# Kernel tuning notes

Hardware: AMD Instinct MI355X
Metric: run time of the kernel (lower is better)

Reference implementation:

```python
import math
import jax, jax.numpy as jnp
import numpy as np

HEAD_DIM = 64


def skew(X):
    # X: (B, M, L). Pad M+1 zeros on last dim, flatten, drop last M, reshape.
    # Shifts row i right by i -> aligns relative positions (adaptive-span trick).
    B, M, L = X.shape
    X = jnp.pad(X, ((0, 0), (0, 0), (0, M + 1)))  # (B, M, L+M+1)
    X = X.reshape(B, -1)[:, :-M].reshape(B, M, M + L)
    return X


def setup_inputs() -> dict:
    key = jax.random.key(0)
    k1, k2, k3, k4 = jax.random.split(key, 4)
    BH, M, D, LIM = 16, 2048, HEAD_DIM, 2048
    return {
        "query": jax.random.normal(k1, (BH, M, D), jnp.float32),
        "key": jax.random.normal(k2, (BH, M, D), jnp.float32),
        "value": jax.random.normal(k3, (BH, M, D), jnp.float32),
        "key_pe": jax.random.normal(k4, (1, D, LIM), jnp.float32),
    }


def reference(query, key, value, key_pe):
    M = query.shape[1]
    Lk = key.shape[1]
    neg_inf = jnp.float32(float("-inf"))
    # causal mask: -inf strictly above diagonal, last M rows
    mask_causal = jnp.triu(jnp.full((Lk, Lk), neg_inf, dtype=query.dtype), k=1)[-M:]
    # content scores: (BH, M, Lk)
    attn = jnp.einsum("bmd,bld->bml", query, key)
    L_size = attn.shape[-1]
    # relative-position scores via skew trick
    attn_pos = jnp.einsum("bmd,xdl->bml", query, key_pe[:, :, -L_size:])
    attn_pos = skew(attn_pos)[:, :, -L_size - 1:-1]
    attn = (attn + attn_pos + mask_causal) / math.sqrt(HEAD_DIM)
    attn = jax.nn.softmax(attn, axis=-1)
    out = jnp.einsum("bml,bld->bmd", attn, value)
    return out  # aux_loss is the constant 0 in the original module
```

## Files before the change

kernel.cpp:

```cpp
#include <hip/hip_runtime.h>
#include <hip/hip_bf16.h>

typedef __attribute__((ext_vector_type(8))) short short8;
typedef __attribute__((ext_vector_type(4))) float f32x4;

#define MFMA16(A, B, C) __builtin_amdgcn_mfma_f32_16x16x32_bf16((A), (B), (C), 0, 0, 0)

#define GL16(gp, lp) __builtin_amdgcn_global_load_lds( \
    (const __attribute__((address_space(1))) void*)(gp), \
    (__attribute__((address_space(3))) void*)(lp), 16, 0, 0)

__device__ __forceinline__ unsigned short bfbits(float f) {
  return __builtin_bit_cast(unsigned short, (__bf16)f);
}

constexpr int BH = 16;
constexpr int Mn = 2048;
constexpr int Dn = 64;
constexpr int LIMn = 2048;
constexpr size_t KF_SHORTS = (size_t)BH * 32 * 8 * 512;
constexpr size_t PE_JROWS = 132;
constexpr size_t PEF_SHORTS = PE_JROWS * 2 * 512;
constexpr int PART_SLOT = 4224;
constexpr int SLOTS_PER_HEAD = 72;

__device__ __forceinline__ int part_offs(int mt) {
  return (mt < 16) ? 2 * (mt - 8) : (mt < 24 ? 16 + 3 * (mt - 16) : 40 + 4 * (mt - 24));
}


__global__ void prep_all(const float* __restrict__ K, const float* __restrict__ V,
                         const float* __restrict__ PE,
                         unsigned short* __restrict__ Kf, unsigned short* __restrict__ Vf,
                         unsigned short* __restrict__ PEf) {
  __shared__ float tA[64 * 64];
  __shared__ float tB[64 * 64];
  const int b = blockIdx.x, tid = threadIdx.x;
  const int w = tid >> 6, lane = tid & 63, g = lane >> 4, q15 = lane & 15;

  if (b < 512) {
    const int bh = b >> 5, lt = b & 31;
    const float* Ks = K + ((size_t)bh * Mn + lt * 64) * Dn;
    const float* Vs = V + ((size_t)bh * Mn + lt * 64) * Dn;
    const int row = tid >> 2, c0 = (tid & 3) * 16;
#pragma unroll
    for (int i = 0; i < 4; ++i) {
      *(float4*)&tA[row * 64 + c0 + 4 * i] = ((const float4*)(Ks + (size_t)row * 64 + c0))[i];
      *(float4*)&tB[row * 64 + c0 + 4 * i] = ((const float4*)(Vs + (size_t)row * 64 + c0))[i];
    }
    __syncthreads();
#pragma unroll
    for (int i = 0; i < 2; ++i) {
      const int f = 2 * w + i, nt = f >> 1, s = f & 1;
      short8 uk, uv;
#pragma unroll
      for (int j = 0; j < 8; ++j) {
        uk[j] = (short)bfbits(tA[(nt * 16 + q15) * 64 + s * 32 + g * 8 + j]);
        uv[j] = (short)bfbits(tB[(s * 32 + g * 8 + j) * 64 + nt * 16 + q15]);
      }
      const size_t base = ((size_t)(bh * 32 + lt) * 8 + f) * 512 + lane * 8;
      *(short8*)&Kf[base] = uk;
      *(short8*)&Vf[base] = uv;
    }
  } else {
    const int pb = b - 512;
    const int c0 = pb * 64;
    const int d = tid >> 2, cc = (tid & 3) * 16;
#pragma unroll
    for (int i = 0; i < 16; ++i) {
      const int c = c0 + cc + i;
      tA[(cc + i) * 64 + d] = (c < LIMn) ? PE[(size_t)d * LIMn + c] : 0.0f;
    }
    __syncthreads();
#pragma unroll
    for (int s = 0; s < 2; ++s) {
      short8 u;
#pragma unroll
      for (int j = 0; j < 8; ++j)
        u[j] = (short)bfbits(tA[(w * 16 + q15) * 64 + s * 32 + g * 8 + j]);
      *(short8*)&PEf[((size_t)(4 * pb + w) * 2 + s) * 512 + lane * 8] = u;
    }
  }
}


__launch_bounds__(256)
__global__ void stair_main(const float* __restrict__ Qg,
                           const unsigned short* __restrict__ Kf,
                           const unsigned short* __restrict__ Vf,
                           const unsigned short* __restrict__ PEf,
                           float* __restrict__ Og,
                           float* __restrict__ Part,
                           int split) {
  __shared__ __align__(16) unsigned short Kbuf[2][2][4096];
  __shared__ __align__(16) unsigned short Vbuf[2][2][4096];
  __shared__ __align__(16) unsigned short Plds[4][2048];

  const int tid = threadIdx.x;
  const int w = tid >> 6, lane = tid & 63, g = lane >> 4, q15 = lane & 15;
  const int bid = blockIdx.x;

  int bh, mt, chunk, t0, t1, nch;
  bh = bid & 15;
  if (split) {
    const int u = bid >> 4;
    if (u < 32)      { mt = 31 - (u >> 2); chunk = u & 3; }
    else if (u < 56) { const int v = u - 32, q = v / 3; mt = 23 - q; chunk = v - q * 3; }
    else if (u < 72) { const int v = u - 56; mt = 15 - (v >> 1); chunk = v & 1; }
    else             { mt = 7 - (u - 72); chunk = 0; }
    t0 = chunk * 8;
    t1 = (t0 + 8 < mt + 1) ? (t0 + 8) : (mt + 1);
    nch = (mt + 8) >> 3;
  } else {
    mt = 31 - (bid >> 4); chunk = 0; t0 = 0; t1 = mt + 1; nch = 1;
  }
  const int m0w = mt * 64 + w * 16;
  const int jb0 = 127 - 4 * mt - w;

  const float* Qb = Qg + (size_t)bh * Mn * Dn;
  float* Ob = Og + (size_t)bh * Mn * Dn;

  short8 aq[2];
  {
    const float* qp = Qb + (size_t)(m0w + q15) * Dn;
#pragma unroll
    for (int s = 0; s < 2; ++s) {
      const float4* p = (const float4*)(qp + s * 32 + g * 8);
      float4 f0 = p[0], f1 = p[1];
      short8 a;
      a[0]=(short)bfbits(f0.x); a[1]=(short)bfbits(f0.y); a[2]=(short)bfbits(f0.z); a[3]=(short)bfbits(f0.w);
      a[4]=(short)bfbits(f1.x); a[5]=(short)bfbits(f1.y); a[6]=(short)bfbits(f1.z); a[7]=(short)bfbits(f1.w);
      aq[s] = a;
    }
  }

  float mrun[4], lp[4];
  f32x4 o[4] = {};
#pragma unroll
  for (int r = 0; r < 4; ++r) { mrun[r] = -1e30f; lp[r] = 0.0f; }

  auto STAGE1 = [&](int b, int slot, int t) {
    const size_t toff = ((size_t)(bh * 32 + t) * 8) * 512;
#pragma unroll
    for (int i = 0; i < 2; ++i) {
      const int f = 2 * w + i;
      const size_t off = toff + (size_t)f * 512 + lane * 8;
      GL16(&Kf[off], &Kbuf[b][slot][f * 512]);
      GL16(&Vf[off], &Vbuf[b][slot][f * 512]);
    }
  };

  auto QK = [&](f32x4 qk[4], int cur, int slot, int ntmax) {
#pragma unroll
    for (int s = 0; s < 2; ++s)
#pragma unroll
      for (int nt = 0; nt < 4; ++nt)
        if (nt <= ntmax) {
          short8 bfr = *(const short8*)&Kbuf[cur][slot][(nt * 2 + s) * 512 + lane * 8];
          qk[nt] = MFMA16(aq[s], bfr, qk[nt]);
        }
  };

  auto GATHER = [&](float sv[4][4], const f32x4 qk[4], const f32x4 ev[5],
                    int ntmax, bool diag) {
#pragma unroll
    for (int nt = 0; nt < 4; ++nt)
      if (nt <= ntmax) {
#pragma unroll
        for (int r = 0; r < 4; ++r) {
          const int rw = g * 4 + r;
          const int srcLane = (lane & 48) | ((q15 + 15 - rw) & 15);
          const bool cond = (((q15 + rw + 1) & 15) > rw);
          const float sel = cond ? ev[nt + 1][r] : ev[nt][r];
          const float er = __shfl(sel, srcLane, 64);
          const int li = nt * 16 + q15;
          const bool masked = diag && (li > w * 16 + rw);
          sv[nt][r] = masked ? -1e30f : (qk[nt][r] + er) * 0.125f;
        }
      }
  };

  auto PV = [&](const float sv[4][4], int cur, int slot, int smax) {
#pragma unroll
    for (int nt = 0; nt < 4; ++nt)
#pragma unroll
      for (int r = 0; r < 4; ++r) {
        const int rw = g * 4 + r;
        Plds[w][slot * 1024 + ((rw * 64 + nt * 16 + q15) ^ ((rw & 7) << 3))] = bfbits(sv[nt][r]);
      }
    short8 pa[2];
#pragma unroll
    for (int s = 0; s < 2; ++s)
      if (s <= smax)
        pa[s] = *(short8*)&Plds[w][slot * 1024 + ((q15 * 64 + s * 32 + g * 8) ^ ((q15 & 7) << 3))];
#pragma unroll
    for (int s = 0; s < 2; ++s)
      if (s <= smax)
#pragma unroll
        for (int nt = 0; nt < 4; ++nt) {
          short8 bfr = *(const short8*)&Vbuf[cur][slot][(nt * 2 + s) * 512 + lane * 8];
          o[nt] = MFMA16(pa[s], bfr, o[nt]);
        }
  };

  auto PAIR = [&](int t, int cur, bool diagB) {
    const int jbA = jb0 + 4 * t;
    const int jbB = jbA + 4;
    const int ntmaxB = diagB ? w : 3;
    const int u5B = diagB ? (w + 2) : 5;
    const int smaxB = diagB ? (w >> 1) : 1;

    short8 peA[2][5], peB[2][5];
#pragma unroll
    for (int s = 0; s < 2; ++s)
#pragma unroll
      for (int u = 0; u < 5; ++u) {
        peA[s][u] = *(const short8*)&PEf[((size_t)(jbA + u) * 2 + s) * 512 + lane * 8];
        if (u < u5B)
          peB[s][u] = *(const short8*)&PEf[((size_t)(jbB + u) * 2 + s) * 512 + lane * 8];
      }

    f32x4 qkA[4] = {}, qkB[4] = {};
    QK(qkA, cur, 0, 3);
    QK(qkB, cur, 1, ntmaxB);

    f32x4 evA[5] = {};
#pragma unroll
    for (int s = 0; s < 2; ++s)
#pragma unroll
      for (int u = 0; u < 5; ++u) evA[u] = MFMA16(aq[s], peA[s][u], evA[u]);

    float svA[4][4], svB[4][4];
#pragma unroll
    for (int nt = 0; nt < 4; ++nt)
#pragma unroll
      for (int r = 0; r < 4; ++r) { svA[nt][r] = -1e30f; svB[nt][r] = -1e30f; }

    GATHER(svA, qkA, evA, 3, false);

    f32x4 evB[5] = {};
#pragma unroll
    for (int s = 0; s < 2; ++s)
#pragma unroll
      for (int u = 0; u < 5; ++u)
        if (u < u5B) evB[u] = MFMA16(aq[s], peB[s][u], evB[u]);

    GATHER(svB, qkB, evB, ntmaxB, diagB);

    float lmax[4];
#pragma unroll
    for (int r = 0; r < 4; ++r) {
      float a = fmaxf(fmaxf(svA[0][r], svA[1][r]), fmaxf(svA[2][r], svA[3][r]));
      float b = fmaxf(fmaxf(svB[0][r], svB[1][r]), fmaxf(svB[2][r], svB[3][r]));
      lmax[r] = fmaxf(a, b);
    }
    const bool fast = __all((lmax[0] <= mrun[0] + 8.f) & (lmax[1] <= mrun[1] + 8.f) &
                            (lmax[2] <= mrun[2] + 8.f) & (lmax[3] <= mrun[3] + 8.f));
    if (!fast) {
#pragma unroll
      for (int r = 0; r < 4; ++r) {
        float mx = lmax[r];
        mx = fmaxf(mx, __shfl_xor(mx, 1));
        mx = fmaxf(mx, __shfl_xor(mx, 2));
        mx = fmaxf(mx, __shfl_xor(mx, 4));
        mx = fmaxf(mx, __shfl_xor(mx, 8));
        const float mn = fmaxf(mrun[r], mx);
        const float alpha = exp2f((mrun[r] - mn) * 1.44269504f);
        mrun[r] = mn;
        lp[r] *= alpha;
        o[0][r] *= alpha; o[1][r] *= alpha; o[2][r] *= alpha; o[3][r] *= alpha;
      }
    }
#pragma unroll
    for (int nt = 0; nt < 4; ++nt)
#pragma unroll
      for (int r = 0; r < 4; ++r) {
        svA[nt][r] = exp2f((svA[nt][r] - mrun[r]) * 1.44269504f);
        svB[nt][r] = exp2f((svB[nt][r] - mrun[r]) * 1.44269504f);
      }
#pragma unroll
    for (int r = 0; r < 4; ++r)
      lp[r] += ((svA[0][r] + svA[1][r]) + (svA[2][r] + svA[3][r])) +
               ((svB[0][r] + svB[1][r]) + (svB[2][r] + svB[3][r]));

    PV(svA, cur, 0, 1);
    PV(svB, cur, 1, smaxB);
  };

  auto SINGLE = [&](int t, int cur, bool diag) {
    const int jb = jb0 + 4 * t;
    const int ntmax = diag ? w : 3;
    const int u5 = diag ? (w + 2) : 5;
    const int smax = diag ? (w >> 1) : 1;

    short8 pe[2][5];
#pragma unroll
    for (int s = 0; s < 2; ++s)
#pragma unroll
      for (int u = 0; u < 5; ++u)
        if (u < u5)
          pe[s][u] = *(const short8*)&PEf[((size_t)(jb + u) * 2 + s) * 512 + lane * 8];

    f32x4 qk[4] = {};
    QK(qk, cur, 0, ntmax);
    f32x4 ev[5] = {};
#pragma unroll
    for (int s = 0; s < 2; ++s)
#pragma unroll
      for (int u = 0; u < 5; ++u)
        if (u < u5) ev[u] = MFMA16(aq[s], pe[s][u], ev[u]);

    float sv[4][4];
#pragma unroll
    for (int nt = 0; nt < 4; ++nt)
#pragma unroll
      for (int r = 0; r < 4; ++r) sv[nt][r] = -1e30f;
    GATHER(sv, qk, ev, ntmax, diag);

    float lmax[4];
#pragma unroll
    for (int r = 0; r < 4; ++r)
      lmax[r] = fmaxf(fmaxf(sv[0][r], sv[1][r]), fmaxf(sv[2][r], sv[3][r]));
    const bool fast = __all((lmax[0] <= mrun[0] + 8.f) & (lmax[1] <= mrun[1] + 8.f) &
                            (lmax[2] <= mrun[2] + 8.f) & (lmax[3] <= mrun[3] + 8.f));
    if (!fast) {
#pragma unroll
      for (int r = 0; r < 4; ++r) {
        float mx = lmax[r];
        mx = fmaxf(mx, __shfl_xor(mx, 1));
        mx = fmaxf(mx, __shfl_xor(mx, 2));
        mx = fmaxf(mx, __shfl_xor(mx, 4));
        mx = fmaxf(mx, __shfl_xor(mx, 8));
        const float mn = fmaxf(mrun[r], mx);
        const float alpha = exp2f((mrun[r] - mn) * 1.44269504f);
        mrun[r] = mn;
        lp[r] *= alpha;
        o[0][r] *= alpha; o[1][r] *= alpha; o[2][r] *= alpha; o[3][r] *= alpha;
      }
    }
#pragma unroll
    for (int nt = 0; nt < 4; ++nt)
#pragma unroll
      for (int r = 0; r < 4; ++r)
// ... 8 lines not shown
    int cur = 0;
    int t = t0;
    const int n0 = (t1 - t0 >= 2) ? 2 : 1;
    STAGE1(0, 0, t0);
    if (n0 == 2) STAGE1(0, 1, t0 + 1);
    __syncthreads();
    while (t < t1) {
      const int n = (t1 - t >= 2) ? 2 : 1;
      const int rem = t1 - (t + n);
      const int nn = (rem >= 2) ? 2 : rem;
      if (nn > 0) {
        STAGE1(cur ^ 1, 0, t + n);
        if (nn == 2) STAGE1(cur ^ 1, 1, t + n + 1);
      }
      if (n == 2) PAIR(t, cur, (t + 1 == mt));
      else SINGLE(t, cur, (t == mt));
      if (nn > 0) __syncthreads();
      cur ^= 1;
      t += n;
    }
  }

  float lr[4];
#pragma unroll
  for (int r = 0; r < 4; ++r) {
    float s = lp[r];
    s += __shfl_xor(s, 1);
    s += __shfl_xor(s, 2);
    s += __shfl_xor(s, 4);
    s += __shfl_xor(s, 8);
    lr[r] = s;
  }

  if (nch == 1) {
#pragma unroll
    for (int nt = 0; nt < 4; ++nt)
#pragma unroll
      for (int r = 0; r < 4; ++r) {
        const int m = m0w + g * 4 + r;
        Ob[(size_t)m * Dn + nt * 16 + q15] = o[nt][r] / lr[r];
      }
  } else {
    float* ps = Part + ((size_t)bh * SLOTS_PER_HEAD + part_offs(mt) + chunk) * PART_SLOT;
#pragma unroll
    for (int nt = 0; nt < 4; ++nt)
#pragma unroll
      for (int r = 0; r < 4; ++r)
        ps[(w * 16 + g * 4 + r) * 64 + nt * 16 + q15] = o[nt][r];
#pragma unroll
    for (int r = 0; r < 4; ++r)
      if (q15 == g * 4 + r) {
        ps[4096 + w * 16 + q15] = mrun[r];
        ps[4160 + w * 16 + q15] = lr[r];
      }
  }
}


__launch_bounds__(256, 4)
__global__ void combine_parts(const float* __restrict__ Part, float* __restrict__ Og) {
  const int bid = blockIdx.x;
  const int bh = bid & 15;
  const int mt = 8 + (bid >> 4);
  const int nch = (mt + 8) >> 3;
  const float* base = Part + ((size_t)bh * SLOTS_PER_HEAD + part_offs(mt)) * PART_SLOT;
  const int tid = threadIdx.x;
  const int row = tid >> 2;
  const int qc = (tid & 3) * 16;

  float mstar = -1e30f;
#pragma unroll
  for (int c = 0; c < 4; ++c)
    if (c < nch) mstar = fmaxf(mstar, base[c * PART_SLOT + 4096 + row]);
  float lsum = 0.f;
  f32x4 acc0 = {}, acc1 = {}, acc2 = {}, acc3 = {};
#pragma unroll
  for (int c = 0; c < 4; ++c)
    if (c < nch) {
      const float* ps = base + c * PART_SLOT;
      const float sc = exp2f((ps[4096 + row] - mstar) * 1.44269504f);
      lsum += ps[4160 + row] * sc;
      const f32x4* op = (const f32x4*)&ps[row * 64 + qc];
      acc0 += op[0] * sc; acc1 += op[1] * sc; acc2 += op[2] * sc; acc3 += op[3] * sc;
    }
  const float inv = 1.f / lsum;
  float* dst = Og + ((size_t)bh * Mn + mt * 64 + row) * Dn + qc;
  *(f32x4*)&dst[0]  = acc0 * inv;
  *(f32x4*)&dst[4]  = acc1 * inv;
  *(f32x4*)&dst[8]  = acc2 * inv;
  *(f32x4*)&dst[12] = acc3 * inv;
}


constexpr int ESTRIDE = 84;

__launch_bounds__(256, 2)
__global__ void stair_attn_fb(const float* __restrict__ Qg,
                              const float* __restrict__ Kg,
                              const float* __restrict__ Vg,
                              const float* __restrict__ PEg,
                              float* __restrict__ Og) {
  __shared__ __align__(16) unsigned short Kb[64 * 64];
  __shared__ __align__(16) unsigned short Vt[64 * 64];
  __shared__ __align__(16) unsigned short Pb[128 * 64];
  __shared__ __align__(16) float Elds[4 * 16 * ESTRIDE];
  __shared__ __align__(16) unsigned short Plds[4 * 16 * 64];

  const int tid = threadIdx.x;
  const int w = tid >> 6;
  const int lane = tid & 63;
  const int g = lane >> 4;
  const int q15 = lane & 15;

  const int bid = blockIdx.x;
  const int bh = bid & 15;
  const int jid = bid >> 4;
  const int mt = (jid < 16) ? (2 * jid) : (63 - 2 * jid);
  const int m0 = mt * 64;

  const float* Qb = Qg + (size_t)bh * Mn * Dn;
  const float* Kbase = Kg + (size_t)bh * Mn * Dn;
  const float* Vbase = Vg + (size_t)bh * Mn * Dn;
  float* Ob = Og + (size_t)bh * Mn * Dn;
// ... 173 lines not shown
    for (int s = 0; s < 2; ++s)
#pragma unroll
      for (int nt = 0; nt < 4; ++nt) {
        int d = nt * 16 + q15;
        short8 b = *(short8*)&Vt[(d * 64 + s * 32 + dso) ^ ((d & 7) << 3)];
        o[nt] = MFMA16(pa[s], b, o[nt]);
      }
  }

#pragma unroll
  for (int nt = 0; nt < 4; ++nt)
#pragma unroll
    for (int r = 0; r < 4; ++r) {
      int m = m0 + 16 * w + g * 4 + r;
      Ob[(size_t)m * Dn + nt * 16 + q15] = o[nt][r] / lrun[r];
    }
}


extern "C" void kernel_launch(void* const* d_in, const int* in_sizes, int n_in,
                              void* d_out, int out_size, void* d_ws, size_t ws_size,
                              hipStream_t stream) {
  (void)in_sizes; (void)n_in; (void)out_size;
  const float* Q  = (const float*)d_in[0];
  const float* K  = (const float*)d_in[1];
  const float* V  = (const float*)d_in[2];
  const float* PE = (const float*)d_in[3];
  float* Out = (float*)d_out;

  const size_t szK = KF_SHORTS * sizeof(unsigned short);
  const size_t szV = szK;
  const size_t szP = PEF_SHORTS * sizeof(unsigned short);
  const size_t szPart = (size_t)BH * SLOTS_PER_HEAD * PART_SLOT * 4;
  const size_t need1 = szK + szV + szP;
  const size_t need2 = need1 + szPart;

  if (ws_size >= need1) {
    unsigned short* Kf  = (unsigned short*)d_ws;
    unsigned short* Vf  = (unsigned short*)((char*)d_ws + szK);
    unsigned short* PEf = (unsigned short*)((char*)d_ws + szK + szV);
    float* Part = (float*)((char*)d_ws + need1);

    hipLaunchKernelGGL(prep_all, dim3(512 + 33), dim3(256), 0, stream, K, V, PE, Kf, Vf, PEf);
    if (ws_size >= need2) {
      hipLaunchKernelGGL(stair_main, dim3(BH * 80), dim3(256), 0, stream,
                         Q, Kf, Vf, PEf, Out, Part, 1);
      hipLaunchKernelGGL(combine_parts, dim3(BH * 24), dim3(256), 0, stream, Part, Out);
    } else {
      hipLaunchKernelGGL(stair_main, dim3(512), dim3(256), 0, stream,
                         Q, Kf, Vf, PEf, Out, (float*)d_ws, 0);
    }
  } else {
    hipLaunchKernelGGL(stair_attn_fb, dim3(512), dim3(256), 0, stream, Q, K, V, PE, Out);
  }
}
```

Before: 75.82 us.

## Precompute skewed positional scores in a separate kernel and stream them as fp16

```diff
diff --git a/kernel.cpp b/kernel.cpp
--- a/kernel.cpp
+++ b/kernel.cpp
@@ -12,6 +12,12 @@
 
 __device__ __forceinline__ unsigned short bfbits(float f) {
   return __builtin_bit_cast(unsigned short, (__bf16)f);
+}
+__device__ __forceinline__ unsigned short h16bits(float f) {
+  return __builtin_bit_cast(unsigned short, (_Float16)f);
+}
+__device__ __forceinline__ float h16val(unsigned short u) {
+  return (float)__builtin_bit_cast(_Float16, u);
 }
 
 constexpr int BH = 16;
@@ -23,6 +29,7 @@
 constexpr size_t PEF_SHORTS = PE_JROWS * 2 * 512;
 constexpr int PART_SLOT = 4224;
 constexpr int SLOTS_PER_HEAD = 72;
+constexpr int TILES_PER_HEAD = 528;
 
 __device__ __forceinline__ int part_offs(int mt) {
   return (mt < 16) ? 2 * (mt - 8) : (mt < 24 ? 16 + 3 * (mt - 16) : 40 + 4 * (mt - 24));
@@ -80,6 +87,351 @@
         u[j] = (short)bfbits(tA[(w * 16 + q15) * 64 + s * 32 + g * 8 + j]);
       *(short8*)&PEf[((size_t)(4 * pb + w) * 2 + s) * 512 + lane * 8] = u;
     }
+  }
+}
+
+
+__launch_bounds__(256)
+__global__ void pos_gemm(const float* __restrict__ Qg,
+                         const unsigned short* __restrict__ PEf,
+                         unsigned short* __restrict__ Spos) {
+  const int tid = threadIdx.x;
+  const int w = tid >> 6, lane = tid & 63, g = lane >> 4, q15 = lane & 15;
+  const int bid = blockIdx.x;
+  const int bh = bid & 15;
+  const int u = bid >> 4;
+  int mt = (int)((sqrtf(8.f * u + 1.f) - 1.f) * 0.5f);
+  while ((mt + 1) * (mt + 2) / 2 <= u) ++mt;
+  while (mt * (mt + 1) / 2 > u) --mt;
+  const int t = u - mt * (mt + 1) / 2;
+  const int m0w = mt * 64 + w * 16;
+  const int jb = 127 - 4 * mt - w + 4 * t;
+
+  short8 aq[2];
+  {
+    const float* qp = Qg + (size_t)bh * Mn * Dn + (size_t)(m0w + q15) * Dn;
+#pragma unroll
+    for (int s = 0; s < 2; ++s) {
+      const float4* p = (const float4*)(qp + s * 32 + g * 8);
+      float4 f0 = p[0], f1 = p[1];
+      short8 a;
+      a[0]=(short)bfbits(f0.x); a[1]=(short)bfbits(f0.y); a[2]=(short)bfbits(f0.z); a[3]=(short)bfbits(f0.w);
+      a[4]=(short)bfbits(f1.x); a[5]=(short)bfbits(f1.y); a[6]=(short)bfbits(f1.z); a[7]=(short)bfbits(f1.w);
+      aq[s] = a;
+    }
+  }
+
+  short8 pe[2][5];
+#pragma unroll
+  for (int s = 0; s < 2; ++s)
+#pragma unroll
+    for (int u5 = 0; u5 < 5; ++u5)
+      pe[s][u5] = *(const short8*)&PEf[((size_t)(jb + u5) * 2 + s) * 512 + lane * 8];
+
+  f32x4 ev[5] = {};
+#pragma unroll
+  for (int s = 0; s < 2; ++s)
+#pragma unroll
+    for (int u5 = 0; u5 < 5; ++u5)
+      ev[u5] = MFMA16(aq[s], pe[s][u5], ev[u5]);
+
+  short8 o0, o1;
+#pragma unroll
+  for (int nt = 0; nt < 4; ++nt)
+#pragma unroll
+    for (int r = 0; r < 4; ++r) {
+      const int rw = g * 4 + r;
+      const int srcLane = (lane & 48) | ((q15 + 15 - rw) & 15);
+      const bool cond = (((q15 + rw + 1) & 15) > rw);
+      const float sel = cond ? ev[nt + 1][r] : ev[nt][r];
+      const float er = __shfl(sel, srcLane, 64);
+      const int idx = nt * 4 + r;
+      if (idx < 8) o0[idx] = (short)h16bits(er);
+      else o1[idx - 8] = (short)h16bits(er);
+    }
+  unsigned short* dst = Spos + (((size_t)(bh * TILES_PER_HEAD + u) * 4 + w) * 64 + lane) * 16;
+  *(short8*)&dst[0] = o0;
+  *(short8*)&dst[8] = o1;
+}
+
+
+__launch_bounds__(256)
+__global__ void stair_main_sp(const float* __restrict__ Qg,
+                              const unsigned short* __restrict__ Kf,
+                              const unsigned short* __restrict__ Vf,
+                              const unsigned short* __restrict__ Spos,
+                              float* __restrict__ Og,
+                              float* __restrict__ Part) {
+  __shared__ __align__(16) unsigned short Kbuf[2][2][4096];
+  __shared__ __align__(16) unsigned short Vbuf[2][2][4096];
+  __shared__ __align__(16) unsigned short Plds[4][2048];
+
+  const int tid = threadIdx.x;
+  const int w = tid >> 6, lane = tid & 63, g = lane >> 4, q15 = lane & 15;
+  const int bid = blockIdx.x;
+
+  int bh, mt, chunk, t0, t1, nch;
+  bh = bid & 15;
+  {
+    const int u = bid >> 4;
+    if (u < 32)      { mt = 31 - (u >> 2); chunk = u & 3; }
+    else if (u < 56) { const int v = u - 32, q = v / 3; mt = 23 - q; chunk = v - q * 3; }
+    else if (u < 72) { const int v = u - 56; mt = 15 - (v >> 1); chunk = v & 1; }
+    else             { mt = 7 - (u - 72); chunk = 0; }
+    t0 = chunk * 8;
+    t1 = (t0 + 8 < mt + 1) ? (t0 + 8) : (mt + 1);
+    nch = (mt + 8) >> 3;
+  }
+  const int m0w = mt * 64 + w * 16;
+  const size_t spBase = ((size_t)bh * TILES_PER_HEAD + (size_t)mt * (mt + 1) / 2);
+
+  const float* Qb = Qg + (size_t)bh * Mn * Dn;
+  float* Ob = Og + (size_t)bh * Mn * Dn;
+
+  short8 aq[2];
+  {
+    const float* qp = Qb + (size_t)(m0w + q15) * Dn;
+#pragma unroll
+    for (int s = 0; s < 2; ++s) {
+      const float4* p = (const float4*)(qp + s * 32 + g * 8);
+      float4 f0 = p[0], f1 = p[1];
+      short8 a;
+      a[0]=(short)bfbits(f0.x); a[1]=(short)bfbits(f0.y); a[2]=(short)bfbits(f0.z); a[3]=(short)bfbits(f0.w);
+      a[4]=(short)bfbits(f1.x); a[5]=(short)bfbits(f1.y); a[6]=(short)bfbits(f1.z); a[7]=(short)bfbits(f1.w);
+      aq[s] = a;
+    }
+  }
+
+  float mrun[4], lp[4];
+  f32x4 o[4] = {};
+#pragma unroll
+  for (int r = 0; r < 4; ++r) { mrun[r] = -1e30f; lp[r] = 0.0f; }
+
+  auto STAGE1 = [&](int b, int slot, int t) {
+    const size_t toff = ((size_t)(bh * 32 + t) * 8) * 512;
+#pragma unroll
+    for (int i = 0; i < 2; ++i) {
+      const int f = 2 * w + i;
+      const size_t off = toff + (size_t)f * 512 + lane * 8;
+      GL16(&Kf[off], &Kbuf[b][slot][f * 512]);
+      GL16(&Vf[off], &Vbuf[b][slot][f * 512]);
+    }
+  };
+
+  auto QK = [&](f32x4 qk[4], int cur, int slot, int ntmax) {
+#pragma unroll
+    for (int s = 0; s < 2; ++s)
+#pragma unroll
+      for (int nt = 0; nt < 4; ++nt)
+        if (nt <= ntmax) {
+          short8 bfr = *(const short8*)&Kbuf[cur][slot][(nt * 2 + s) * 512 + lane * 8];
+          qk[nt] = MFMA16(aq[s], bfr, qk[nt]);
+        }
+  };
+
+  auto PV = [&](const float sv[4][4], int cur, int slot, int smax) {
+#pragma unroll
+    for (int nt = 0; nt < 4; ++nt)
+#pragma unroll
+      for (int r = 0; r < 4; ++r) {
+        const int rw = g * 4 + r;
+        Plds[w][slot * 1024 + ((rw * 64 + nt * 16 + q15) ^ ((rw & 7) << 3))] = bfbits(sv[nt][r]);
+      }
+    short8 pa[2];
+#pragma unroll
+    for (int s = 0; s < 2; ++s)
+      if (s <= smax)
+        pa[s] = *(short8*)&Plds[w][slot * 1024 + ((q15 * 64 + s * 32 + g * 8) ^ ((q15 & 7) << 3))];
+#pragma unroll
+    for (int s = 0; s < 2; ++s)
+      if (s <= smax)
+#pragma unroll
+        for (int nt = 0; nt < 4; ++nt) {
+          short8 bfr = *(const short8*)&Vbuf[cur][slot][(nt * 2 + s) * 512 + lane * 8];
+          o[nt] = MFMA16(pa[s], bfr, o[nt]);
+        }
+  };
+
+  auto PAIR = [&](int t, int cur, bool diagB) {
+    const int ntmaxB = diagB ? w : 3;
+    const int smaxB = diagB ? (w >> 1) : 1;
+
+    const unsigned short* spA = Spos + (((spBase + t) * 4 + w) * 64 + lane) * 16;
+    short8 eA0 = *(const short8*)&spA[0];
+    short8 eA1 = *(const short8*)&spA[8];
+    short8 eB0 = *(const short8*)&spA[4096];
+    short8 eB1 = *(const short8*)&spA[4096 + 8];
+
+    f32x4 qkA[4] = {}, qkB[4] = {};
+    QK(qkA, cur, 0, 3);
+    QK(qkB, cur, 1, ntmaxB);
+
+    float svA[4][4], svB[4][4];
+#pragma unroll
+    for (int nt = 0; nt < 4; ++nt)
+#pragma unroll
+      for (int r = 0; r < 4; ++r) {
+        const int rw = g * 4 + r;
+        const int li = nt * 16 + q15;
+        const int idx = nt * 4 + r;
+        const float eAf = h16val((unsigned short)(idx < 8 ? eA0[idx] : eA1[idx - 8]));
+        const float eBf = h16val((unsigned short)(idx < 8 ? eB0[idx] : eB1[idx - 8]));
+        svA[nt][r] = (qkA[nt][r] + eAf) * 0.125f;
+        const bool maskedB = (nt > ntmaxB) || (diagB && (li > w * 16 + rw));
+        svB[nt][r] = maskedB ? -1e30f : (qkB[nt][r] + eBf) * 0.125f;
+      }
+
+    float lmax[4];
+#pragma unroll
+    for (int r = 0; r < 4; ++r) {
+      float a = fmaxf(fmaxf(svA[0][r], svA[1][r]), fmaxf(svA[2][r], svA[3][r]));
+      float b = fmaxf(fmaxf(svB[0][r], svB[1][r]), fmaxf(svB[2][r], svB[3][r]));
+      lmax[r] = fmaxf(a, b);
+    }
+    const bool fast = __all((lmax[0] <= mrun[0] + 8.f) & (lmax[1] <= mrun[1] + 8.f) &
+                            (lmax[2] <= mrun[2] + 8.f) & (lmax[3] <= mrun[3] + 8.f));
+    if (!fast) {
+#pragma unroll
+      for (int r = 0; r < 4; ++r) {
+        float mx = lmax[r];
+        mx = fmaxf(mx, __shfl_xor(mx, 1));
+        mx = fmaxf(mx, __shfl_xor(mx, 2));
+        mx = fmaxf(mx, __shfl_xor(mx, 4));
+        mx = fmaxf(mx, __shfl_xor(mx, 8));
+        const float mn = fmaxf(mrun[r], mx);
+        const float alpha = exp2f((mrun[r] - mn) * 1.44269504f);
+        mrun[r] = mn;
+        lp[r] *= alpha;
+        o[0][r] *= alpha; o[1][r] *= alpha; o[2][r] *= alpha; o[3][r] *= alpha;
+      }
+    }
+#pragma unroll
+    for (int nt = 0; nt < 4; ++nt)
+#pragma unroll
+      for (int r = 0; r < 4; ++r) {
+        svA[nt][r] = exp2f((svA[nt][r] - mrun[r]) * 1.44269504f);
+        svB[nt][r] = exp2f((svB[nt][r] - mrun[r]) * 1.44269504f);
+      }
+#pragma unroll
+    for (int r = 0; r < 4; ++r)
+      lp[r] += ((svA[0][r] + svA[1][r]) + (svA[2][r] + svA[3][r])) +
+               ((svB[0][r] + svB[1][r]) + (svB[2][r] + svB[3][r]));
+
+    PV(svA, cur, 0, 1);
+    PV(svB, cur, 1, smaxB);
+  };
+
+  auto SINGLE = [&](int t, int cur, bool diag) {
+    const int ntmax = diag ? w : 3;
+    const int smax = diag ? (w >> 1) : 1;
+
+    const unsigned short* sp = Spos + (((spBase + t) * 4 + w) * 64 + lane) * 16;
+    short8 e0 = *(const short8*)&sp[0];
+    short8 e1 = *(const short8*)&sp[8];
+
+    f32x4 qk[4] = {};
+    QK(qk, cur, 0, ntmax);
+
+    float sv[4][4];
+#pragma unroll
+    for (int nt = 0; nt < 4; ++nt)
+#pragma unroll
+      for (int r = 0; r < 4; ++r) {
+        const int rw = g * 4 + r;
+        const int li = nt * 16 + q15;
+        const int idx = nt * 4 + r;
+        const float ef = h16val((unsigned short)(idx < 8 ? e0[idx] : e1[idx - 8]));
+        const bool masked = (nt > ntmax) || (diag && (li > w * 16 + rw));
+        sv[nt][r] = masked ? -1e30f : (qk[nt][r] + ef) * 0.125f;
+      }
+
+    float lmax[4];
+#pragma unroll
+    for (int r = 0; r < 4; ++r)
+      lmax[r] = fmaxf(fmaxf(sv[0][r], sv[1][r]), fmaxf(sv[2][r], sv[3][r]));
+    const bool fast = __all((lmax[0] <= mrun[0] + 8.f) & (lmax[1] <= mrun[1] + 8.f) &
+                            (lmax[2] <= mrun[2] + 8.f) & (lmax[3] <= mrun[3] + 8.f));
+    if (!fast) {
+#pragma unroll
+      for (int r = 0; r < 4; ++r) {
+        float mx = lmax[r];
+        mx = fmaxf(mx, __shfl_xor(mx, 1));
+        mx = fmaxf(mx, __shfl_xor(mx, 2));
+        mx = fmaxf(mx, __shfl_xor(mx, 4));
+        mx = fmaxf(mx, __shfl_xor(mx, 8));
+        const float mn = fmaxf(mrun[r], mx);
+        const float alpha = exp2f((mrun[r] - mn) * 1.44269504f);
+        mrun[r] = mn;
+        lp[r] *= alpha;
+        o[0][r] *= alpha; o[1][r] *= alpha; o[2][r] *= alpha; o[3][r] *= alpha;
+      }
+    }
+#pragma unroll
+    for (int nt = 0; nt < 4; ++nt)
+#pragma unroll
+      for (int r = 0; r < 4; ++r)
+        sv[nt][r] = exp2f((sv[nt][r] - mrun[r]) * 1.44269504f);
+#pragma unroll
+    for (int r = 0; r < 4; ++r)
+      lp[r] += (sv[0][r] + sv[1][r]) + (sv[2][r] + sv[3][r]);
+    PV(sv, cur, 0, smax);
+  };
+
+  {
+    int cur = 0;
+    int t = t0;
+    const int n0 = (t1 - t0 >= 2) ? 2 : 1;
+    STAGE1(0, 0, t0);
+    if (n0 == 2) STAGE1(0, 1, t0 + 1);
+    __syncthreads();
+    while (t < t1) {
+      const int n = (t1 - t >= 2) ? 2 : 1;
+      const int rem = t1 - (t + n);
+      const int nn = (rem >= 2) ? 2 : rem;
+      if (nn > 0) {
+        STAGE1(cur ^ 1, 0, t + n);
+        if (nn == 2) STAGE1(cur ^ 1, 1, t + n + 1);
+      }
+      if (n == 2) PAIR(t, cur, (t + 1 == mt));
+      else SINGLE(t, cur, (t == mt));
+      if (nn > 0) __syncthreads();
+      cur ^= 1;
+      t += n;
+    }
+  }
+
+  float lr[4];
+#pragma unroll
+  for (int r = 0; r < 4; ++r) {
+    float s = lp[r];
+    s += __shfl_xor(s, 1);
+    s += __shfl_xor(s, 2);
+    s += __shfl_xor(s, 4);
+    s += __shfl_xor(s, 8);
+    lr[r] = s;
+  }
+
+  if (nch == 1) {
+#pragma unroll
+    for (int nt = 0; nt < 4; ++nt)
+#pragma unroll
+      for (int r = 0; r < 4; ++r) {
+        const int m = m0w + g * 4 + r;
+        Ob[(size_t)m * Dn + nt * 16 + q15] = o[nt][r] / lr[r];
+      }
+  } else {
+    float* ps = Part + ((size_t)bh * SLOTS_PER_HEAD + part_offs(mt) + chunk) * PART_SLOT;
+#pragma unroll
+    for (int nt = 0; nt < 4; ++nt)
+#pragma unroll
+      for (int r = 0; r < 4; ++r)
+        ps[(w * 16 + g * 4 + r) * 64 + nt * 16 + q15] = o[nt][r];
+#pragma unroll
+    for (int r = 0; r < 4; ++r)
+      if (q15 == g * 4 + r) {
+        ps[4096 + w * 16 + q15] = mrun[r];
+        ps[4160 + w * 16 + q15] = lr[r];
+      }
   }
 }
 
@@ -679,17 +1031,25 @@
   const size_t szV = szK;
   const size_t szP = PEF_SHORTS * sizeof(unsigned short);
   const size_t szPart = (size_t)BH * SLOTS_PER_HEAD * PART_SLOT * 4;
+  const size_t szSpos = (size_t)BH * TILES_PER_HEAD * 4096 * 2;
   const size_t need1 = szK + szV + szP;
   const size_t need2 = need1 + szPart;
+  const size_t need3 = need2 + szSpos;
 
   if (ws_size >= need1) {
     unsigned short* Kf  = (unsigned short*)d_ws;
     unsigned short* Vf  = (unsigned short*)((char*)d_ws + szK);
     unsigned short* PEf = (unsigned short*)((char*)d_ws + szK + szV);
     float* Part = (float*)((char*)d_ws + need1);
+    unsigned short* Spos = (unsigned short*)((char*)d_ws + need2);
 
     hipLaunchKernelGGL(prep_all, dim3(512 + 33), dim3(256), 0, stream, K, V, PE, Kf, Vf, PEf);
-    if (ws_size >= need2) {
+    if (ws_size >= need3) {
+      hipLaunchKernelGGL(pos_gemm, dim3(BH * TILES_PER_HEAD), dim3(256), 0, stream, Q, PEf, Spos);
+      hipLaunchKernelGGL(stair_main_sp, dim3(BH * 80), dim3(256), 0, stream,
+                         Q, Kf, Vf, Spos, Out, Part);
+      hipLaunchKernelGGL(combine_parts, dim3(BH * 24), dim3(256), 0, stream, Part, Out);
+    } else if (ws_size >= need2) {
       hipLaunchKernelGGL(stair_main, dim3(BH * 80), dim3(256), 0, stream,
                          Q, Kf, Vf, PEf, Out, Part, 1);
       hipLaunchKernelGGL(combine_parts, dim3(BH * 24), dim3(256), 0, stream, Part, Out);
```

Measured after the change: 95.12 us. 25.5% more time.

## Process two adjacent query tiles per 512-thread block sharing staged K/V

Applied to the files above, without the earlier changes.

```diff
diff --git a/kernel.cpp b/kernel.cpp
--- a/kernel.cpp
+++ b/kernel.cpp
@@ -54,9 +54,9 @@
       const int f = 2 * w + i, nt = f >> 1, s = f & 1;
       short8 uk, uv;
 #pragma unroll
-      for (int j = 0; j < 8; ++j) {
-        uk[j] = (short)bfbits(tA[(nt * 16 + q15) * 64 + s * 32 + g * 8 + j]);
-        uv[j] = (short)bfbits(tB[(s * 32 + g * 8 + j) * 64 + nt * 16 + q15]);
+      for (int jj = 0; jj < 8; ++jj) {
+        uk[jj] = (short)bfbits(tA[(nt * 16 + q15) * 64 + s * 32 + g * 8 + jj]);
+        uv[jj] = (short)bfbits(tB[(s * 32 + g * 8 + jj) * 64 + nt * 16 + q15]);
       }
       const size_t base = ((size_t)(bh * 32 + lt) * 8 + f) * 512 + lane * 8;
       *(short8*)&Kf[base] = uk;
@@ -68,54 +68,51 @@
     const int d = tid >> 2, cc = (tid & 3) * 16;
 #pragma unroll
     for (int i = 0; i < 16; ++i) {
-      const int c = c0 + cc + i;
-      tA[(cc + i) * 64 + d] = (c < LIMn) ? PE[(size_t)d * LIMn + c] : 0.0f;
+      const int cx = c0 + cc + i;
+      tA[(cc + i) * 64 + d] = (cx < LIMn) ? PE[(size_t)d * LIMn + cx] : 0.0f;
     }
     __syncthreads();
 #pragma unroll
     for (int s = 0; s < 2; ++s) {
-      short8 u;
-#pragma unroll
-      for (int j = 0; j < 8; ++j)
-        u[j] = (short)bfbits(tA[(w * 16 + q15) * 64 + s * 32 + g * 8 + j]);
-      *(short8*)&PEf[((size_t)(4 * pb + w) * 2 + s) * 512 + lane * 8] = u;
+      short8 uu;
+#pragma unroll
+      for (int jj = 0; jj < 8; ++jj)
+        uu[jj] = (short)bfbits(tA[(w * 16 + q15) * 64 + s * 32 + g * 8 + jj]);
+      *(short8*)&PEf[((size_t)(4 * pb + w) * 2 + s) * 512 + lane * 8] = uu;
     }
   }
 }
 
 
-__launch_bounds__(256)
-__global__ void stair_main(const float* __restrict__ Qg,
-                           const unsigned short* __restrict__ Kf,
-                           const unsigned short* __restrict__ Vf,
-                           const unsigned short* __restrict__ PEf,
-                           float* __restrict__ Og,
-                           float* __restrict__ Part,
-                           int split) {
+__launch_bounds__(512, 4)
+__global__ void stair_main8(const float* __restrict__ Qg,
+                            const unsigned short* __restrict__ Kf,
+                            const unsigned short* __restrict__ Vf,
+                            const unsigned short* __restrict__ PEf,
+                            float* __restrict__ Og,
+                            float* __restrict__ Part) {
   __shared__ __align__(16) unsigned short Kbuf[2][2][4096];
   __shared__ __align__(16) unsigned short Vbuf[2][2][4096];
-  __shared__ __align__(16) unsigned short Plds[4][2048];
+  __shared__ __align__(16) unsigned short Plds[8][1024];
 
   const int tid = threadIdx.x;
   const int w = tid >> 6, lane = tid & 63, g = lane >> 4, q15 = lane & 15;
   const int bid = blockIdx.x;
-
-  int bh, mt, chunk, t0, t1, nch;
-  bh = bid & 15;
-  if (split) {
-    const int u = bid >> 4;
-    if (u < 32)      { mt = 31 - (u >> 2); chunk = u & 3; }
-    else if (u < 56) { const int v = u - 32, q = v / 3; mt = 23 - q; chunk = v - q * 3; }
-    else if (u < 72) { const int v = u - 56; mt = 15 - (v >> 1); chunk = v & 1; }
-    else             { mt = 7 - (u - 72); chunk = 0; }
-    t0 = chunk * 8;
-    t1 = (t0 + 8 < mt + 1) ? (t0 + 8) : (mt + 1);
-    nch = (mt + 8) >> 3;
-  } else {
-    mt = 31 - (bid >> 4); chunk = 0; t0 = 0; t1 = mt + 1; nch = 1;
-  }
-  const int m0w = mt * 64 + w * 16;
-  const int jb0 = 127 - 4 * mt - w;
+  const int bh = bid & 15;
+  const int u = bid >> 4;
+  int j, c;
+  if (u < 16)      { j = 15 - (u >> 2); c = u & 3; }
+  else if (u < 28) { const int v = u - 16; const int q = v / 3; j = 11 - q; c = v - q * 3; }
+  else if (u < 36) { const int v = u - 28; j = 7 - (v >> 1); c = v & 1; }
+  else             { j = 3 - (u - 36); c = 0; }
+  const int ma = 2 * j, mb = ma + 1;
+  const int t0 = 8 * c;
+  const int t1 = (8 * c + 8 < mb + 1) ? (8 * c + 8) : (mb + 1);
+  const int nch = (mb + 8) >> 3;
+  const int w4 = w & 3;
+  const int myMt = (w >= 4) ? mb : ma;
+  const int m0w = myMt * 64 + w4 * 16;
+  const int jb0 = 127 - 4 * myMt - w4;
 
   const float* Qb = Qg + (size_t)bh * Mn * Dn;
   float* Ob = Og + (size_t)bh * Mn * Dn;
@@ -140,14 +137,9 @@
   for (int r = 0; r < 4; ++r) { mrun[r] = -1e30f; lp[r] = 0.0f; }
 
   auto STAGE1 = [&](int b, int slot, int t) {
-    const size_t toff = ((size_t)(bh * 32 + t) * 8) * 512;
-#pragma unroll
-    for (int i = 0; i < 2; ++i) {
-      const int f = 2 * w + i;
-      const size_t off = toff + (size_t)f * 512 + lane * 8;
-      GL16(&Kf[off], &Kbuf[b][slot][f * 512]);
-      GL16(&Vf[off], &Vbuf[b][slot][f * 512]);
-    }
+    const size_t off = ((size_t)(bh * 32 + t) * 8 + w) * 512 + (size_t)lane * 8;
+    GL16(&Kf[off], &Kbuf[b][slot][w * 512]);
+    GL16(&Vf[off], &Vbuf[b][slot][w * 512]);
   };
 
   auto QK = [&](f32x4 qk[4], int cur, int slot, int ntmax) {
@@ -174,7 +166,7 @@
           const float sel = cond ? ev[nt + 1][r] : ev[nt][r];
           const float er = __shfl(sel, srcLane, 64);
           const int li = nt * 16 + q15;
-          const bool masked = diag && (li > w * 16 + rw);
+          const bool masked = diag && (li > w4 * 16 + rw);
           sv[nt][r] = masked ? -1e30f : (qk[nt][r] + er) * 0.125f;
         }
       }
@@ -186,13 +178,13 @@
 #pragma unroll
       for (int r = 0; r < 4; ++r) {
         const int rw = g * 4 + r;
-        Plds[w][slot * 1024 + ((rw * 64 + nt * 16 + q15) ^ ((rw & 7) << 3))] = bfbits(sv[nt][r]);
+        Plds[w][(rw * 64 + nt * 16 + q15) ^ ((rw & 7) << 3)] = bfbits(sv[nt][r]);
       }
     short8 pa[2];
 #pragma unroll
     for (int s = 0; s < 2; ++s)
       if (s <= smax)
-        pa[s] = *(short8*)&Plds[w][slot * 1024 + ((q15 * 64 + s * 32 + g * 8) ^ ((q15 & 7) << 3))];
+        pa[s] = *(short8*)&Plds[w][(q15 * 64 + s * 32 + g * 8) ^ ((q15 & 7) << 3)];
 #pragma unroll
     for (int s = 0; s < 2; ++s)
       if (s <= smax)
@@ -203,32 +195,38 @@
         }
   };
 
-  auto PAIR = [&](int t, int cur, bool diagB) {
+  auto PAIR = [&](int t, int cur) {
+    const int tB = t + 1;
+    const bool diagA = (t == myMt);
+    const bool actB  = (tB <= myMt);
+    const bool diagB = (tB == myMt);
+    const int ntmaxA = diagA ? w4 : 3;
+    const int smaxA  = diagA ? (w4 >> 1) : 1;
+    const int ntmaxB = actB ? (diagB ? w4 : 3) : -1;
+    const int u5B    = actB ? (diagB ? (w4 + 2) : 5) : 0;
+    const int smaxB  = actB ? (diagB ? (w4 >> 1) : 1) : -1;
     const int jbA = jb0 + 4 * t;
     const int jbB = jbA + 4;
-    const int ntmaxB = diagB ? w : 3;
-    const int u5B = diagB ? (w + 2) : 5;
-    const int smaxB = diagB ? (w >> 1) : 1;
 
     short8 peA[2][5], peB[2][5];
 #pragma unroll
     for (int s = 0; s < 2; ++s)
 #pragma unroll
-      for (int u = 0; u < 5; ++u) {
-        peA[s][u] = *(const short8*)&PEf[((size_t)(jbA + u) * 2 + s) * 512 + lane * 8];
-        if (u < u5B)
-          peB[s][u] = *(const short8*)&PEf[((size_t)(jbB + u) * 2 + s) * 512 + lane * 8];
+      for (int uu = 0; uu < 5; ++uu) {
+        peA[s][uu] = *(const short8*)&PEf[((size_t)(jbA + uu) * 2 + s) * 512 + lane * 8];
+        if (uu < u5B)
+          peB[s][uu] = *(const short8*)&PEf[((size_t)(jbB + uu) * 2 + s) * 512 + lane * 8];
       }
 
     f32x4 qkA[4] = {}, qkB[4] = {};
-    QK(qkA, cur, 0, 3);
+    QK(qkA, cur, 0, ntmaxA);
     QK(qkB, cur, 1, ntmaxB);
 
     f32x4 evA[5] = {};
 #pragma unroll
     for (int s = 0; s < 2; ++s)
 #pragma unroll
-      for (int u = 0; u < 5; ++u) evA[u] = MFMA16(aq[s], peA[s][u], evA[u]);
+      for (int uu = 0; uu < 5; ++uu) evA[uu] = MFMA16(aq[s], peA[s][uu], evA[uu]);
 
     float svA[4][4], svB[4][4];
 #pragma unroll
@@ -236,14 +234,14 @@
 #pragma unroll
       for (int r = 0; r < 4; ++r) { svA[nt][r] = -1e30f; svB[nt][r] = -1e30f; }
 
-    GATHER(svA, qkA, evA, 3, false);
+    GATHER(svA, qkA, evA, ntmaxA, diagA);
 
     f32x4 evB[5] = {};
 #pragma unroll
     for (int s = 0; s < 2; ++s)
 #pragma unroll
-      for (int u = 0; u < 5; ++u)
-        if (u < u5B) evB[u] = MFMA16(aq[s], peB[s][u], evB[u]);
+      for (int uu = 0; uu < 5; ++uu)
+        if (uu < u5B) evB[uu] = MFMA16(aq[s], peB[s][uu], evB[uu]);
 
     GATHER(svB, qkB, evB, ntmaxB, diagB);
 
@@ -283,6 +281,283 @@
       lp[r] += ((svA[0][r] + svA[1][r]) + (svA[2][r] + svA[3][r])) +
                ((svB[0][r] + svB[1][r]) + (svB[2][r] + svB[3][r]));
 
+    PV(svA, cur, 0, smaxA);
+    PV(svB, cur, 1, smaxB);
+  };
+
+  {
+    int cur = 0;
+    STAGE1(0, 0, t0);
+    STAGE1(0, 1, t0 + 1);
+    __syncthreads();
+    for (int t = t0; t < t1; t += 2) {
+      const bool more = (t + 2 < t1);
+      if (more) {
+        STAGE1(cur ^ 1, 0, t + 2);
+        STAGE1(cur ^ 1, 1, t + 3);
+      }
+      PAIR(t, cur);
+      if (more) __syncthreads();
+      cur ^= 1;
+    }
+  }
+
+  float lr[4];
+#pragma unroll
+  for (int r = 0; r < 4; ++r) {
+    float s = lp[r];
+    s += __shfl_xor(s, 1);
+    s += __shfl_xor(s, 2);
+    s += __shfl_xor(s, 4);
+    s += __shfl_xor(s, 8);
+    lr[r] = s;
+  }
+
+  if (nch == 1) {
+#pragma unroll
+    for (int nt = 0; nt < 4; ++nt)
+#pragma unroll
+      for (int r = 0; r < 4; ++r) {
+        const int m = m0w + g * 4 + r;
+        Ob[(size_t)m * Dn + nt * 16 + q15] = o[nt][r] / lr[r];
+      }
+  } else {
+    float* ps = Part + ((size_t)bh * SLOTS_PER_HEAD + part_offs(myMt) + c) * PART_SLOT;
+#pragma unroll
+    for (int nt = 0; nt < 4; ++nt)
+#pragma unroll
+      for (int r = 0; r < 4; ++r)
+        ps[(w4 * 16 + g * 4 + r) * 64 + nt * 16 + q15] = o[nt][r];
+#pragma unroll
+    for (int r = 0; r < 4; ++r)
+      if (q15 == g * 4 + r) {
+        ps[4096 + w4 * 16 + q15] = mrun[r];
+        ps[4160 + w4 * 16 + q15] = lr[r];
+      }
+  }
+}
+
+
+__launch_bounds__(256, 4)
+__global__ void combine_parts(const float* __restrict__ Part, float* __restrict__ Og) {
+  const int bid = blockIdx.x;
+  const int bh = bid & 15;
+  const int mt = 8 + (bid >> 4);
+  const int nch = (mt + 8) >> 3;
+  const float* base = Part + ((size_t)bh * SLOTS_PER_HEAD + part_offs(mt)) * PART_SLOT;
+  const int tid = threadIdx.x;
+  const int row = tid >> 2;
+  const int qc = (tid & 3) * 16;
+
+  float mstar = -1e30f;
+#pragma unroll
+  for (int cc = 0; cc < 4; ++cc)
+    if (cc < nch) mstar = fmaxf(mstar, base[cc * PART_SLOT + 4096 + row]);
+  float lsum = 0.f;
+  f32x4 acc0 = {}, acc1 = {}, acc2 = {}, acc3 = {};
+#pragma unroll
+  for (int cc = 0; cc < 4; ++cc)
+    if (cc < nch) {
+      const float* ps = base + cc * PART_SLOT;
+      const float sc = exp2f((ps[4096 + row] - mstar) * 1.44269504f);
+      lsum += ps[4160 + row] * sc;
+      const f32x4* op = (const f32x4*)&ps[row * 64 + qc];
+      acc0 += op[0] * sc; acc1 += op[1] * sc; acc2 += op[2] * sc; acc3 += op[3] * sc;
+    }
+  const float inv = 1.f / lsum;
+  float* dst = Og + ((size_t)bh * Mn + mt * 64 + row) * Dn + qc;
+  *(f32x4*)&dst[0]  = acc0 * inv;
+  *(f32x4*)&dst[4]  = acc1 * inv;
+  *(f32x4*)&dst[8]  = acc2 * inv;
+  *(f32x4*)&dst[12] = acc3 * inv;
+}
+
+
+__launch_bounds__(256)
+__global__ void stair_main(const float* __restrict__ Qg,
+                           const unsigned short* __restrict__ Kf,
+                           const unsigned short* __restrict__ Vf,
+                           const unsigned short* __restrict__ PEf,
+                           float* __restrict__ Og) {
+  __shared__ __align__(16) unsigned short Kbuf[2][2][4096];
+  __shared__ __align__(16) unsigned short Vbuf[2][2][4096];
+  __shared__ __align__(16) unsigned short Plds[4][2048];
+
+  const int tid = threadIdx.x;
+  const int w = tid >> 6, lane = tid & 63, g = lane >> 4, q15 = lane & 15;
+  const int bid = blockIdx.x;
+  const int bh = bid & 15;
+  const int mt = 31 - (bid >> 4);
+  const int t0 = 0, t1 = mt + 1;
+  const int m0w = mt * 64 + w * 16;
+  const int jb0 = 127 - 4 * mt - w;
+
+  const float* Qb = Qg + (size_t)bh * Mn * Dn;
+  float* Ob = Og + (size_t)bh * Mn * Dn;
+
+  short8 aq[2];
+  {
+    const float* qp = Qb + (size_t)(m0w + q15) * Dn;
+#pragma unroll
+    for (int s = 0; s < 2; ++s) {
+      const float4* p = (const float4*)(qp + s * 32 + g * 8);
+      float4 f0 = p[0], f1 = p[1];
+      short8 a;
+      a[0]=(short)bfbits(f0.x); a[1]=(short)bfbits(f0.y); a[2]=(short)bfbits(f0.z); a[3]=(short)bfbits(f0.w);
+      a[4]=(short)bfbits(f1.x); a[5]=(short)bfbits(f1.y); a[6]=(short)bfbits(f1.z); a[7]=(short)bfbits(f1.w);
+      aq[s] = a;
+    }
+  }
+
+  float mrun[4], lp[4];
+  f32x4 o[4] = {};
+#pragma unroll
+  for (int r = 0; r < 4; ++r) { mrun[r] = -1e30f; lp[r] = 0.0f; }
+
+  auto STAGE1 = [&](int b, int slot, int t) {
+    const size_t toff = ((size_t)(bh * 32 + t) * 8) * 512;
+#pragma unroll
+    for (int i = 0; i < 2; ++i) {
+      const int f = 2 * w + i;
+      const size_t off = toff + (size_t)f * 512 + lane * 8;
+      GL16(&Kf[off], &Kbuf[b][slot][f * 512]);
+      GL16(&Vf[off], &Vbuf[b][slot][f * 512]);
+    }
+  };
+
+  auto QK = [&](f32x4 qk[4], int cur, int slot, int ntmax) {
+#pragma unroll
+    for (int s = 0; s < 2; ++s)
+#pragma unroll
+      for (int nt = 0; nt < 4; ++nt)
+        if (nt <= ntmax) {
+          short8 bfr = *(const short8*)&Kbuf[cur][slot][(nt * 2 + s) * 512 + lane * 8];
+          qk[nt] = MFMA16(aq[s], bfr, qk[nt]);
+        }
+  };
+
+  auto GATHER = [&](float sv[4][4], const f32x4 qk[4], const f32x4 ev[5],
+                    int ntmax, bool diag) {
+#pragma unroll
+    for (int nt = 0; nt < 4; ++nt)
+      if (nt <= ntmax) {
+#pragma unroll
+        for (int r = 0; r < 4; ++r) {
+          const int rw = g * 4 + r;
+          const int srcLane = (lane & 48) | ((q15 + 15 - rw) & 15);
+          const bool cond = (((q15 + rw + 1) & 15) > rw);
+          const float sel = cond ? ev[nt + 1][r] : ev[nt][r];
+          const float er = __shfl(sel, srcLane, 64);
+          const int li = nt * 16 + q15;
+          const bool masked = diag && (li > w * 16 + rw);
+          sv[nt][r] = masked ? -1e30f : (qk[nt][r] + er) * 0.125f;
+        }
+      }
+  };
+
+  auto PV = [&](const float sv[4][4], int cur, int slot, int smax) {
+#pragma unroll
+    for (int nt = 0; nt < 4; ++nt)
+#pragma unroll
+      for (int r = 0; r < 4; ++r) {
+        const int rw = g * 4 + r;
+        Plds[w][slot * 1024 + ((rw * 64 + nt * 16 + q15) ^ ((rw & 7) << 3))] = bfbits(sv[nt][r]);
+      }
+    short8 pa[2];
+#pragma unroll
+    for (int s = 0; s < 2; ++s)
+      if (s <= smax)
+        pa[s] = *(short8*)&Plds[w][slot * 1024 + ((q15 * 64 + s * 32 + g * 8) ^ ((q15 & 7) << 3))];
+#pragma unroll
+    for (int s = 0; s < 2; ++s)
+      if (s <= smax)
+#pragma unroll
+        for (int nt = 0; nt < 4; ++nt) {
+          short8 bfr = *(const short8*)&Vbuf[cur][slot][(nt * 2 + s) * 512 + lane * 8];
+          o[nt] = MFMA16(pa[s], bfr, o[nt]);
+        }
+  };
+
+  auto PAIR = [&](int t, int cur, bool diagB) {
+    const int jbA = jb0 + 4 * t;
+    const int jbB = jbA + 4;
+    const int ntmaxB = diagB ? w : 3;
+    const int u5B = diagB ? (w + 2) : 5;
+    const int smaxB = diagB ? (w >> 1) : 1;
+
+    short8 peA[2][5], peB[2][5];
+#pragma unroll
+    for (int s = 0; s < 2; ++s)
+#pragma unroll
+      for (int uu = 0; uu < 5; ++uu) {
+        peA[s][uu] = *(const short8*)&PEf[((size_t)(jbA + uu) * 2 + s) * 512 + lane * 8];
+        if (uu < u5B)
+          peB[s][uu] = *(const short8*)&PEf[((size_t)(jbB + uu) * 2 + s) * 512 + lane * 8];
+      }
+
+    f32x4 qkA[4] = {}, qkB[4] = {};
+    QK(qkA, cur, 0, 3);
+    QK(qkB, cur, 1, ntmaxB);
+
+    f32x4 evA[5] = {};
+#pragma unroll
+    for (int s = 0; s < 2; ++s)
+#pragma unroll
+      for (int uu = 0; uu < 5; ++uu) evA[uu] = MFMA16(aq[s], peA[s][uu], evA[uu]);
+
+    float svA[4][4], svB[4][4];
+#pragma unroll
+    for (int nt = 0; nt < 4; ++nt)
+#pragma unroll
+      for (int r = 0; r < 4; ++r) { svA[nt][r] = -1e30f; svB[nt][r] = -1e30f; }
+
+    GATHER(svA, qkA, evA, 3, false);
+
+    f32x4 evB[5] = {};
+#pragma unroll
+    for (int s = 0; s < 2; ++s)
+#pragma unroll
+      for (int uu = 0; uu < 5; ++uu)
+        if (uu < u5B) evB[uu] = MFMA16(aq[s], peB[s][uu], evB[uu]);
+
+    GATHER(svB, qkB, evB, ntmaxB, diagB);
+
+    float lmax[4];
+#pragma unroll
+    for (int r = 0; r < 4; ++r) {
+      float a = fmaxf(fmaxf(svA[0][r], svA[1][r]), fmaxf(svA[2][r], svA[3][r]));
+      float b = fmaxf(fmaxf(svB[0][r], svB[1][r]), fmaxf(svB[2][r], svB[3][r]));
+      lmax[r] = fmaxf(a, b);
+    }
+    const bool fast = __all((lmax[0] <= mrun[0] + 8.f) & (lmax[1] <= mrun[1] + 8.f) &
+                            (lmax[2] <= mrun[2] + 8.f) & (lmax[3] <= mrun[3] + 8.f));
+    if (!fast) {
+#pragma unroll
+      for (int r = 0; r < 4; ++r) {
+        float mx = lmax[r];
+        mx = fmaxf(mx, __shfl_xor(mx, 1));
+        mx = fmaxf(mx, __shfl_xor(mx, 2));
+        mx = fmaxf(mx, __shfl_xor(mx, 4));
+        mx = fmaxf(mx, __shfl_xor(mx, 8));
+        const float mn = fmaxf(mrun[r], mx);
+        const float alpha = exp2f((mrun[r] - mn) * 1.44269504f);
+        mrun[r] = mn;
+        lp[r] *= alpha;
+        o[0][r] *= alpha; o[1][r] *= alpha; o[2][r] *= alpha; o[3][r] *= alpha;
+      }
+    }
+#pragma unroll
+    for (int nt = 0; nt < 4; ++nt)
+#pragma unroll
+      for (int r = 0; r < 4; ++r) {
+        svA[nt][r] = exp2f((svA[nt][r] - mrun[r]) * 1.44269504f);
+        svB[nt][r] = exp2f((svB[nt][r] - mrun[r]) * 1.44269504f);
+      }
+#pragma unroll
+    for (int r = 0; r < 4; ++r)
+      lp[r] += ((svA[0][r] + svA[1][r]) + (svA[2][r] + svA[3][r])) +
+               ((svB[0][r] + svB[1][r]) + (svB[2][r] + svB[3][r]));
+
     PV(svA, cur, 0, 1);
     PV(svB, cur, 1, smaxB);
   };
@@ -297,9 +572,9 @@
 #pragma unroll
     for (int s = 0; s < 2; ++s)
 #pragma unroll
-      for (int u = 0; u < 5; ++u)
-        if (u < u5)
-          pe[s][u] = *(const short8*)&PEf[((size_t)(jb + u) * 2 + s) * 512 + lane * 8];
+      for (int uu = 0; uu < 5; ++uu)
+        if (uu < u5)
+          pe[s][uu] = *(const short8*)&PEf[((size_t)(jb + uu) * 2 + s) * 512 + lane * 8];
 
     f32x4 qk[4] = {};
     QK(qk, cur, 0, ntmax);
@@ -307,8 +582,8 @@
 #pragma unroll
     for (int s = 0; s < 2; ++s)
 #pragma unroll
-      for (int u = 0; u < 5; ++u)
-        if (u < u5) ev[u] = MFMA16(aq[s], pe[s][u], ev[u]);
+      for (int uu = 0; uu < 5; ++uu)
+        if (uu < u5) ev[uu] = MFMA16(aq[s], pe[s][uu], ev[uu]);
 
     float sv[4][4];
 #pragma unroll
@@ -383,63 +658,13 @@
     lr[r] = s;
   }
 
-  if (nch == 1) {
-#pragma unroll
-    for (int nt = 0; nt < 4; ++nt)
-#pragma unroll
-      for (int r = 0; r < 4; ++r) {
-        const int m = m0w + g * 4 + r;
-        Ob[(size_t)m * Dn + nt * 16 + q15] = o[nt][r] / lr[r];
-      }
-  } else {
-    float* ps = Part + ((size_t)bh * SLOTS_PER_HEAD + part_offs(mt) + chunk) * PART_SLOT;
-#pragma unroll
-    for (int nt = 0; nt < 4; ++nt)
-#pragma unroll
-      for (int r = 0; r < 4; ++r)
-        ps[(w * 16 + g * 4 + r) * 64 + nt * 16 + q15] = o[nt][r];
-#pragma unroll
-    for (int r = 0; r < 4; ++r)
-      if (q15 == g * 4 + r) {
-        ps[4096 + w * 16 + q15] = mrun[r];
-        ps[4160 + w * 16 + q15] = lr[r];
-      }
-  }
-}
-
-
-__launch_bounds__(256, 4)
-__global__ void combine_parts(const float* __restrict__ Part, float* __restrict__ Og) {
-  const int bid = blockIdx.x;
-  const int bh = bid & 15;
-  const int mt = 8 + (bid >> 4);
-  const int nch = (mt + 8) >> 3;
-  const float* base = Part + ((size_t)bh * SLOTS_PER_HEAD + part_offs(mt)) * PART_SLOT;
-  const int tid = threadIdx.x;
-  const int row = tid >> 2;
-  const int qc = (tid & 3) * 16;
-
-  float mstar = -1e30f;
-#pragma unroll
-  for (int c = 0; c < 4; ++c)
-    if (c < nch) mstar = fmaxf(mstar, base[c * PART_SLOT + 4096 + row]);
-  float lsum = 0.f;
-  f32x4 acc0 = {}, acc1 = {}, acc2 = {}, acc3 = {};
-#pragma unroll
-  for (int c = 0; c < 4; ++c)
-    if (c < nch) {
-      const float* ps = base + c * PART_SLOT;
-      const float sc = exp2f((ps[4096 + row] - mstar) * 1.44269504f);
-      lsum += ps[4160 + row] * sc;
-      const f32x4* op = (const f32x4*)&ps[row * 64 + qc];
-      acc0 += op[0] * sc; acc1 += op[1] * sc; acc2 += op[2] * sc; acc3 += op[3] * sc;
-    }
-  const float inv = 1.f / lsum;
-  float* dst = Og + ((size_t)bh * Mn + mt * 64 + row) * Dn + qc;
-  *(f32x4*)&dst[0]  = acc0 * inv;
-  *(f32x4*)&dst[4]  = acc1 * inv;
-  *(f32x4*)&dst[8]  = acc2 * inv;
-  *(f32x4*)&dst[12] = acc3 * inv;
+#pragma unroll
+  for (int nt = 0; nt < 4; ++nt)
+#pragma unroll
+    for (int r = 0; r < 4; ++r) {
+      const int m = m0w + g * 4 + r;
+      Ob[(size_t)m * Dn + nt * 16 + q15] = o[nt][r] / lr[r];
+    }
 }
 
 
@@ -690,12 +915,12 @@
 
     hipLaunchKernelGGL(prep_all, dim3(512 + 33), dim3(256), 0, stream, K, V, PE, Kf, Vf, PEf);
     if (ws_size >= need2) {
-      hipLaunchKernelGGL(stair_main, dim3(BH * 80), dim3(256), 0, stream,
-                         Q, Kf, Vf, PEf, Out, Part, 1);
+      hipLaunchKernelGGL(stair_main8, dim3(BH * 40), dim3(512), 0, stream,
+                         Q, Kf, Vf, PEf, Out, Part);
       hipLaunchKernelGGL(combine_parts, dim3(BH * 24), dim3(256), 0, stream, Part, Out);
     } else {
       hipLaunchKernelGGL(stair_main, dim3(512), dim3(256), 0, stream,
-                         Q, Kf, Vf, PEf, Out, (float*)d_ws, 0);
+                         Q, Kf, Vf, PEf, Out);
     }
   } else {
     hipLaunchKernelGGL(stair_attn_fb, dim3(512), dim3(256), 0, stream, Q, K, V, PE, Out);
```

Result: slower. 229.8 us (+203.0%).
